# Kernel tuning notes

Hardware: AMD Instinct MI355X
Metric: run time of the kernel (lower is better)

Reference implementation:

```python
import jax, jax.numpy as jnp
import numpy as np

EPS = 1e-7  # keras backend epsilon
ROUTINGS = 3

def squash(s, axis=-1):
    # v = ||s||^2/(1+||s||^2) * s/||s||
    sq = jnp.sum(jnp.square(s), axis=axis, keepdims=True)
    scale = sq / (1.0 + sq) / jnp.sqrt(sq + EPS)
    return scale * s

def setup_inputs() -> dict:
    key = jax.random.key(0)
    k1, k2 = jax.random.split(key)
    B, in_num, in_dim = 64, 2048, 16
    num_caps, dim_caps = 64, 32
    inputs = jax.random.normal(k1, (B, in_num, in_dim), dtype=jnp.float32)
    # glorot_uniform limit = sqrt(6/(fan_in+fan_out)) with fan_in=in_dim, fan_out=dim_caps
    limit = np.sqrt(6.0 / (in_dim + dim_caps)).astype(np.float32)
    W = jax.random.uniform(k2, (num_caps, in_num, dim_caps, in_dim),
                           dtype=jnp.float32, minval=-limit, maxval=limit)
    return {"inputs": inputs, "W": W}

def reference(inputs, W):
    # inputs: [b, i, l]; W: [j, i, k, l]
    # inputs_hat[b, j, i, k] = W[j, i, k, :] @ inputs[b, i, :]
    u_hat = jnp.einsum('jikl,bil->bjik', W, inputs)
    B, J, I, K = u_hat.shape
    b = jnp.zeros((B, J, I), dtype=u_hat.dtype)  # routing logits
    v = None
    for r in range(ROUTINGS):
        c = jax.nn.softmax(b, axis=1)                      # softmax over output capsules j
        s = jnp.einsum('bji,bjik->bjk', c, u_hat)          # weighted sum over input capsules
        v = squash(s)                                      # [b, j, k]
        if r < ROUTINGS - 1:
            b = b + jnp.einsum('bjk,bjik->bji', v, u_hat)  # agreement update
    return v  # [B, num_capsule, dim_capsule]
```

## Files before the change

kernel.cpp:

```cpp
#include <hip/hip_runtime.h>


#define B_ 64
#define I_ 2048
#define L_ 16
#define J_ 64
#define K_ 32
#define N_ 2048

typedef _Float16 half8_t __attribute__((ext_vector_type(8)));
typedef float f32x16 __attribute__((ext_vector_type(16)));
typedef float float4_t __attribute__((ext_vector_type(4)));

__device__ __forceinline__ f32x16 fzero16() {
    f32x16 z;
#pragma unroll
    for (int r = 0; r < 16; ++r) z[r] = 0.f;
    return z;
}

__global__ __launch_bounds__(256) void cast_x_kernel(const float* __restrict__ X,
                                                     _Float16* __restrict__ Xh) {
    unsigned tid = blockIdx.x * 256u + threadIdx.x;
    unsigned b = tid & 63u;
    unsigned i = tid >> 6;
    const float4_t* src = (const float4_t*)(X + (size_t)(b * I_ + i) * L_);
    float4_t f0 = src[0], f1 = src[1], f2 = src[2], f3 = src[3];
    half8_t h0, h1;
#pragma unroll
    for (int e = 0; e < 4; ++e) {
        h0[e] = (_Float16)f0[e];
        h0[4 + e] = (_Float16)f1[e];
        h1[e] = (_Float16)f2[e];
        h1[4 + e] = (_Float16)f3[e];
    }
    _Float16* dst = Xh + (size_t)(i * B_ + b) * L_;
    *(half8_t*)dst = h0;
    *(half8_t*)(dst + 8) = h1;
}

__global__ __launch_bounds__(512) void s0_cast_kernel(const float* __restrict__ Wf,
                                                      _Float16* __restrict__ Wh_out,
                                                      const _Float16* __restrict__ Xh,
                                                      _Float16* __restrict__ parts,
                                                      int SCH, int ICH) {
    const int tid = threadIdx.x;
    const int w = tid >> 6;
    const int l = tid & 63;
    const int h2 = l >> 5;
    const int kb = l & 31;
    const int chunk = blockIdx.x >> 3;
    const int jq = blockIdx.x & 7;
    const int j = jq * 8 + w;

    float s0[16], s1[16];
#pragma unroll
    for (int r = 0; r < 16; ++r) { s0[r] = 0.f; s1[r] = 0.f; }

    const int i0 = chunk * ICH;
    for (int ii = 0; ii < ICH; ++ii) {
        const int i = i0 + ii;
        const _Float16* xb = Xh + (size_t)i * (B_ * L_);
        half8_t xf0 = *(const half8_t*)(xb + kb * L_ + 8 * h2);
        half8_t xf1 = *(const half8_t*)(xb + (32 + kb) * L_ + 8 * h2);
        const float4_t* wsrc =
            (const float4_t*)(Wf + ((size_t)(j * I_ + i) * K_ + kb) * L_ + 8 * h2);
        float4_t a0 = wsrc[0], a1 = wsrc[1];
        half8_t af;
#pragma unroll
        for (int e = 0; e < 4; ++e) {
            af[e] = (_Float16)a0[e];
            af[4 + e] = (_Float16)a1[e];
        }
        *(half8_t*)(Wh_out + ((size_t)(i * J_ + j) * K_ + kb) * L_ + 8 * h2) = af;
        f32x16 acc0 = __builtin_amdgcn_mfma_f32_32x32x16_f16(af, xf0, fzero16(), 0, 0, 0);
        f32x16 acc1 = __builtin_amdgcn_mfma_f32_32x32x16_f16(af, xf1, fzero16(), 0, 0, 0);
#pragma unroll
        for (int r = 0; r < 16; ++r) {
            s0[r] += acc0[r];
            s1[r] += acc1[r];
        }
    }
#pragma unroll
    for (int r = 0; r < 16; ++r) {
        const int k = (r & 3) + 8 * (r >> 2) + 4 * h2;
        _Float16* p = parts + (((size_t)chunk * J_ + j) * K_ + k) * B_;
        p[kb] = (_Float16)s0[r];
        p[32 + kb] = (_Float16)s1[r];
    }
}

__global__ __launch_bounds__(512) void zcalc_kernel(const _Float16* __restrict__ Wh,
                                                    const _Float16* __restrict__ Xh,
                                                    const _Float16* __restrict__ wvz,
                                                    _Float16* __restrict__ ebuf,
                                                    int SCH, int ICH) {
    const int tid = threadIdx.x;
    const int w = tid >> 6;
    const int l = tid & 63;
    const int h2 = l >> 5;
    const int kb = l & 31;
    const int chunk = blockIdx.x >> 3;
    const int jq = blockIdx.x & 7;
    const int j = jq * 8 + w;

    const _Float16* wp = wvz + ((size_t)(j * 2 + h2) * B_ + kb) * 16;
    const half8_t wv00 = *(const half8_t*)wp;
    const half8_t wv01 = *(const half8_t*)(wp + 8);
    const half8_t wv10 = *(const half8_t*)(wp + 512);
    const half8_t wv11 = *(const half8_t*)(wp + 520);

    const int i0 = chunk * ICH;
    for (int ig = 0; ig < ICH; ig += 4) {
        half8_t af[4], x0[4], x1[4];
#pragma unroll
        for (int q = 0; q < 4; ++q) {
            const int i = i0 + ig + q;
            const _Float16* xb = Xh + (size_t)i * (B_ * L_);
            x0[q] = *(const half8_t*)(xb + kb * L_ + 8 * h2);
            x1[q] = *(const half8_t*)(xb + (32 + kb) * L_ + 8 * h2);
            af[q] = *(const half8_t*)(Wh + ((size_t)(i * J_ + j) * K_ + kb) * L_ + 8 * h2);
        }
#pragma unroll
        for (int q = 0; q < 4; ++q) {
            const int i = i0 + ig + q;
            f32x16 acc0 = __builtin_amdgcn_mfma_f32_32x32x16_f16(af[q], x0[q], fzero16(), 0, 0, 0);
            f32x16 acc1 = __builtin_amdgcn_mfma_f32_32x32x16_f16(af[q], x1[q], fzero16(), 0, 0, 0);
            float z0a = 0.f, z0b = 0.f, z0c = 0.f, z0d = 0.f;
            float z1a = 0.f, z1b = 0.f, z1c = 0.f, z1d = 0.f;
#pragma unroll
            for (int r = 0; r < 4; ++r) {
                z0a += acc0[r]      * (float)wv00[r];
                z0b += acc0[r + 4]  * (float)wv00[r + 4];
                z0c += acc0[r + 8]  * (float)wv01[r];
                z0d += acc0[r + 12] * (float)wv01[r + 4];
                z1a += acc1[r]      * (float)wv10[r];
                z1b += acc1[r + 4]  * (float)wv10[r + 4];
                z1c += acc1[r + 8]  * (float)wv11[r];
                z1d += acc1[r + 12] * (float)wv11[r + 4];
            }
            float z0 = (z0a + z0b) + (z0c + z0d);
            float z1 = (z1a + z1b) + (z1c + z1d);
            z0 += __shfl_xor(z0, 32, 64);
            z1 += __shfl_xor(z1, 32, 64);
            const float zf = fminf((l < 32) ? z0 : z1, 11.0f);
            ebuf[((size_t)j * I_ + i) * B_ + l] = (_Float16)__expf(zf);
        }
    }
}

__global__ __launch_bounds__(256) void dsum_kernel(const _Float16* __restrict__ ebuf,
                                                   float* __restrict__ rD) {
    const int w = threadIdx.x >> 6;
    const int l = threadIdx.x & 63;
    const int i = blockIdx.x * 4 + w;
    float p0 = 0.f, p1 = 0.f, p2 = 0.f, p3 = 0.f;
#pragma unroll
    for (int jq = 0; jq < 16; ++jq) {
        p0 += (float)ebuf[((size_t)(jq * 4 + 0) * I_ + i) * B_ + l];
        p1 += (float)ebuf[((size_t)(jq * 4 + 1) * I_ + i) * B_ + l];
        p2 += (float)ebuf[((size_t)(jq * 4 + 2) * I_ + i) * B_ + l];
        p3 += (float)ebuf[((size_t)(jq * 4 + 3) * I_ + i) * B_ + l];
    }
    rD[i * B_ + l] = 1.0f / ((p0 + p1) + (p2 + p3));
}

__global__ __launch_bounds__(512) void s_kernel(const _Float16* __restrict__ Wh,
                                                const _Float16* __restrict__ Xh,
                                                const _Float16* __restrict__ ebuf,
                                                const float* __restrict__ rD,
                                                _Float16* __restrict__ parts,
                                                int SCH, int ICH) {
    const int tid = threadIdx.x;
    const int w = tid >> 6;
    const int l = tid & 63;
    const int h2 = l >> 5;
    const int kb = l & 31;
    const int chunk = blockIdx.x >> 3;
    const int jq = blockIdx.x & 7;
    const int j = jq * 8 + w;

    float s0[16], s1[16];
#pragma unroll
    for (int r = 0; r < 16; ++r) { s0[r] = 0.f; s1[r] = 0.f; }

    const int i0 = chunk * ICH;
    for (int ig = 0; ig < ICH; ig += 4) {
        half8_t af[4], x0[4], x1[4];
        float e0[4], e1[4], d0[4], d1[4];
#pragma unroll
        for (int q = 0; q < 4; ++q) {
            const int i = i0 + ig + q;
            const _Float16* xb = Xh + (size_t)i * (B_ * L_);
            x0[q] = *(const half8_t*)(xb + kb * L_ + 8 * h2);
            x1[q] = *(const half8_t*)(xb + (32 + kb) * L_ + 8 * h2);
            af[q] = *(const half8_t*)(Wh + ((size_t)(i * J_ + j) * K_ + kb) * L_ + 8 * h2);
            const _Float16* ep = ebuf + ((size_t)j * I_ + i) * B_;
            e0[q] = (float)ep[kb];
            e1[q] = (float)ep[32 + kb];
            d0[q] = rD[i * B_ + kb];
            d1[q] = rD[i * B_ + 32 + kb];
        }
#pragma unroll
        for (int q = 0; q < 4; ++q) {
            f32x16 acc0 = __builtin_amdgcn_mfma_f32_32x32x16_f16(af[q], x0[q], fzero16(), 0, 0, 0);
            f32x16 acc1 = __builtin_amdgcn_mfma_f32_32x32x16_f16(af[q], x1[q], fzero16(), 0, 0, 0);
            const float c0 = e0[q] * d0[q];
            const float c1 = e1[q] * d1[q];
#pragma unroll
            for (int r = 0; r < 16; ++r) {
                s0[r] += c0 * acc0[r];
                s1[r] += c1 * acc1[r];
            }
        }
    }
#pragma unroll
    for (int r = 0; r < 16; ++r) {
        const int k = (r & 3) + 8 * (r >> 2) + 4 * h2;
        _Float16* p = parts + (((size_t)chunk * J_ + j) * K_ + k) * B_;
        p[kb] = (_Float16)s0[r];
        p[32 + kb] = (_Float16)s1[r];
    }
}

__global__ __launch_bounds__(512) void reduce_kernel(const _Float16* __restrict__ parts,
                                                     _Float16* __restrict__ wvz,
                                                     float* __restrict__ out,
                                                     int SCH, int STEP) {
    __shared__ float ssql[8][64];
    const int j = blockIdx.x;
    const int t = threadIdx.x;
    const int b = t & 63;
    const int kg = t >> 6;

    float acc[4] = {0.f, 0.f, 0.f, 0.f};
    for (int ch = 0; ch < SCH; ++ch) {
        const _Float16* p = parts + (((size_t)ch * J_ + j) * K_ + kg * 4) * B_ + b;
#pragma unroll
        for (int q = 0; q < 4; ++q) acc[q] += (float)p[(size_t)q * B_];
    }
    if (STEP == 0) {
#pragma unroll
        for (int q = 0; q < 4; ++q) acc[q] *= (1.0f / 64.0f);
    }
    ssql[kg][b] = acc[0] * acc[0] + acc[1] * acc[1] + acc[2] * acc[2] + acc[3] * acc[3];
    __syncthreads();
    float sq = 0.f;
#pragma unroll
    for (int g = 0; g < 8; ++g) sq += ssql[g][b];
    const float scale = sq / (1.0f + sq) / sqrtf(sq + 1e-7f);

    if (STEP == 2) {
#pragma unroll
        for (int q = 0; q < 4; ++q)
            out[(size_t)b * N_ + j * K_ + kg * 4 + q] = acc[q] * scale;
    } else {
        _Float16* wp = wvz + ((size_t)(j * 2 + (kg & 1)) * B_ + b) * 16 + 4 * (kg >> 1);
#pragma unroll
        for (int q = 0; q < 4; ++q) {
            const float prev = (STEP == 0) ? 0.f : (float)wp[q];
            wp[q] = (_Float16)(prev + acc[q] * scale);
        }
    }
}

extern "C" void kernel_launch(void* const* d_in, const int* in_sizes, int n_in,
                              void* d_out, int out_size, void* d_ws, size_t ws_size,
                              hipStream_t stream) {
    const float* X = (const float*)d_in[0];
    const float* W = (const float*)d_in[1];
    float* out = (float*)d_out;
    char* ws = (char*)d_ws;

    const size_t WH_BYTES = (size_t)I_ * J_ * K_ * L_ * 2;
    const size_t XH_BYTES = (size_t)I_ * B_ * L_ * 2;
    const size_t WVZ_BYTES = (size_t)J_ * 2 * B_ * 16 * 2;
    const size_t EB_BYTES = (size_t)J_ * I_ * B_ * 2;
    const size_t RD_BYTES = (size_t)I_ * B_ * 4;
    const size_t FIX = WH_BYTES + XH_BYTES + WVZ_BYTES + EB_BYTES + RD_BYTES;

    int SCH = 64;
    if (ws_size < FIX + (size_t)64 * N_ * B_ * 2) SCH = 32;
    if (ws_size < FIX + (size_t)32 * N_ * B_ * 2) SCH = 16;
    const int ICH = I_ / SCH;

    _Float16* Wh = (_Float16*)ws;
    _Float16* Xh = (_Float16*)(ws + WH_BYTES);
    _Float16* wvz = (_Float16*)(ws + WH_BYTES + XH_BYTES);
    _Float16* ebuf = (_Float16*)(ws + WH_BYTES + XH_BYTES + WVZ_BYTES);
    float* rD = (float*)(ws + WH_BYTES + XH_BYTES + WVZ_BYTES + EB_BYTES);
    _Float16* parts = (_Float16*)(ws + FIX);

    cast_x_kernel<<<dim3((B_ * I_) / 256), dim3(256), 0, stream>>>(X, Xh);

    s0_cast_kernel<<<dim3(SCH * 8), dim3(512), 0, stream>>>(W, Wh, Xh, parts, SCH, ICH);
    reduce_kernel<<<dim3(J_), dim3(512), 0, stream>>>(parts, wvz, out, SCH, 0);

    zcalc_kernel<<<dim3(SCH * 8), dim3(512), 0, stream>>>(Wh, Xh, wvz, ebuf, SCH, ICH);
    dsum_kernel<<<dim3(I_ / 4), dim3(256), 0, stream>>>(ebuf, rD);
    s_kernel<<<dim3(SCH * 8), dim3(512), 0, stream>>>(Wh, Xh, ebuf, rD, parts, SCH, ICH);
    reduce_kernel<<<dim3(J_), dim3(512), 0, stream>>>(parts, wvz, out, SCH, 1);

    zcalc_kernel<<<dim3(SCH * 8), dim3(512), 0, stream>>>(Wh, Xh, wvz, ebuf, SCH, ICH);
    dsum_kernel<<<dim3(I_ / 4), dim3(256), 0, stream>>>(ebuf, rD);
    s_kernel<<<dim3(SCH * 8), dim3(512), 0, stream>>>(Wh, Xh, ebuf, rD, parts, SCH, ICH);
    reduce_kernel<<<dim3(J_), dim3(512), 0, stream>>>(parts, wvz, out, SCH, 2);

    (void)in_sizes; (void)n_in; (void)out_size;
}
```

Baseline: 297.9 us.

## Fuse logit, softmax denominator and normalization into one per-input-block kernel

Replaces the separate zcalc and dsum kernels with one kernel. Each block owns 4 input capsules across all 64 output capsules, keeps exp(logits) in LDS, reduces the softmax denominator there, and writes normalized coefficients c. The s kernel then reads c directly instead of reading e and the reciprocal denominator separately. This removes one launch per routing step, a full re-read of the exp buffer, and the rD buffer traffic, at the cost of a 32KB LDS tile and a different grid shape that may lower occupancy.

```diff
diff --git a/kernel.cpp b/kernel.cpp
--- a/kernel.cpp
+++ b/kernel.cpp
@@ -90,42 +90,41 @@
     }
 }
 
-__global__ __launch_bounds__(512) void zcalc_kernel(const _Float16* __restrict__ Wh,
-                                                    const _Float16* __restrict__ Xh,
-                                                    const _Float16* __restrict__ wvz,
-                                                    _Float16* __restrict__ ebuf,
-                                                    int SCH, int ICH) {
+__global__ __launch_bounds__(512) void zsm2_kernel(const _Float16* __restrict__ Wh,
+                                                   const _Float16* __restrict__ Xh,
+                                                   const _Float16* __restrict__ wvz,
+                                                   _Float16* __restrict__ cbuf) {
+    __shared__ _Float16 elds[J_ * 4 * B_];
+    __shared__ float rdl[4 * B_];
     const int tid = threadIdx.x;
     const int w = tid >> 6;
     const int l = tid & 63;
     const int h2 = l >> 5;
     const int kb = l & 31;
-    const int chunk = blockIdx.x >> 3;
-    const int jq = blockIdx.x & 7;
-    const int j = jq * 8 + w;
-
-    const _Float16* wp = wvz + ((size_t)(j * 2 + h2) * B_ + kb) * 16;
-    const half8_t wv00 = *(const half8_t*)wp;
-    const half8_t wv01 = *(const half8_t*)(wp + 8);
-    const half8_t wv10 = *(const half8_t*)(wp + 512);
-    const half8_t wv11 = *(const half8_t*)(wp + 520);
-
-    const int i0 = chunk * ICH;
-    for (int ig = 0; ig < ICH; ig += 4) {
-        half8_t af[4], x0[4], x1[4];
-#pragma unroll
-        for (int q = 0; q < 4; ++q) {
-            const int i = i0 + ig + q;
-            const _Float16* xb = Xh + (size_t)i * (B_ * L_);
-            x0[q] = *(const half8_t*)(xb + kb * L_ + 8 * h2);
-            x1[q] = *(const half8_t*)(xb + (32 + kb) * L_ + 8 * h2);
-            af[q] = *(const half8_t*)(Wh + ((size_t)(i * J_ + j) * K_ + kb) * L_ + 8 * h2);
-        }
-#pragma unroll
-        for (int q = 0; q < 4; ++q) {
-            const int i = i0 + ig + q;
-            f32x16 acc0 = __builtin_amdgcn_mfma_f32_32x32x16_f16(af[q], x0[q], fzero16(), 0, 0, 0);
-            f32x16 acc1 = __builtin_amdgcn_mfma_f32_32x32x16_f16(af[q], x1[q], fzero16(), 0, 0, 0);
+    const int i0 = blockIdx.x * 4;
+
+    half8_t xf0[4], xf1[4];
+#pragma unroll
+    for (int ii = 0; ii < 4; ++ii) {
+        const _Float16* xb = Xh + (size_t)(i0 + ii) * (B_ * L_);
+        xf0[ii] = *(const half8_t*)(xb + kb * L_ + 8 * h2);
+        xf1[ii] = *(const half8_t*)(xb + (32 + kb) * L_ + 8 * h2);
+    }
+
+#pragma unroll
+    for (int jj = 0; jj < 8; ++jj) {
+        const int j = w * 8 + jj;
+        const _Float16* wp = wvz + ((size_t)(j * 2 + h2) * B_ + kb) * 16;
+        const half8_t wv00 = *(const half8_t*)wp;
+        const half8_t wv01 = *(const half8_t*)(wp + 8);
+        const half8_t wv10 = *(const half8_t*)(wp + 512);
+        const half8_t wv11 = *(const half8_t*)(wp + 520);
+#pragma unroll
+        for (int ii = 0; ii < 4; ++ii) {
+            half8_t af = *(const half8_t*)(Wh +
+                ((size_t)((i0 + ii) * J_ + j) * K_ + kb) * L_ + 8 * h2);
+            f32x16 acc0 = __builtin_amdgcn_mfma_f32_32x32x16_f16(af, xf0[ii], fzero16(), 0, 0, 0);
+            f32x16 acc1 = __builtin_amdgcn_mfma_f32_32x32x16_f16(af, xf1[ii], fzero16(), 0, 0, 0);
             float z0a = 0.f, z0b = 0.f, z0c = 0.f, z0d = 0.f;
             float z1a = 0.f, z1b = 0.f, z1c = 0.f, z1d = 0.f;
 #pragma unroll
@@ -144,31 +143,38 @@
             z0 += __shfl_xor(z0, 32, 64);
             z1 += __shfl_xor(z1, 32, 64);
             const float zf = fminf((l < 32) ? z0 : z1, 11.0f);
-            ebuf[((size_t)j * I_ + i) * B_ + l] = (_Float16)__expf(zf);
-        }
-    }
-}
-
-__global__ __launch_bounds__(256) void dsum_kernel(const _Float16* __restrict__ ebuf,
-                                                   float* __restrict__ rD) {
-    const int w = threadIdx.x >> 6;
-    const int l = threadIdx.x & 63;
-    const int i = blockIdx.x * 4 + w;
-    float p0 = 0.f, p1 = 0.f, p2 = 0.f, p3 = 0.f;
-#pragma unroll
-    for (int jq = 0; jq < 16; ++jq) {
-        p0 += (float)ebuf[((size_t)(jq * 4 + 0) * I_ + i) * B_ + l];
-        p1 += (float)ebuf[((size_t)(jq * 4 + 1) * I_ + i) * B_ + l];
-        p2 += (float)ebuf[((size_t)(jq * 4 + 2) * I_ + i) * B_ + l];
-        p3 += (float)ebuf[((size_t)(jq * 4 + 3) * I_ + i) * B_ + l];
-    }
-    rD[i * B_ + l] = 1.0f / ((p0 + p1) + (p2 + p3));
+            elds[((size_t)j * 4 + ii) * B_ + l] = (_Float16)__expf(zf);
+        }
+    }
+    __syncthreads();
+
+    if (w < 4) {
+        float p0 = 0.f, p1 = 0.f, p2 = 0.f, p3 = 0.f;
+#pragma unroll
+        for (int jq = 0; jq < 16; ++jq) {
+            p0 += (float)elds[((size_t)(jq * 4 + 0) * 4 + w) * B_ + l];
+            p1 += (float)elds[((size_t)(jq * 4 + 1) * 4 + w) * B_ + l];
+            p2 += (float)elds[((size_t)(jq * 4 + 2) * 4 + w) * B_ + l];
+            p3 += (float)elds[((size_t)(jq * 4 + 3) * 4 + w) * B_ + l];
+        }
+        rdl[w * B_ + l] = 1.0f / ((p0 + p1) + (p2 + p3));
+    }
+    __syncthreads();
+
+#pragma unroll
+    for (int jj = 0; jj < 8; ++jj) {
+        const int j = w * 8 + jj;
+#pragma unroll
+        for (int ii = 0; ii < 4; ++ii) {
+            const float c = (float)elds[((size_t)j * 4 + ii) * B_ + l] * rdl[ii * B_ + l];
+            cbuf[((size_t)j * I_ + (i0 + ii)) * B_ + l] = (_Float16)c;
+        }
+    }
 }
 
 __global__ __launch_bounds__(512) void s_kernel(const _Float16* __restrict__ Wh,
                                                 const _Float16* __restrict__ Xh,
-                                                const _Float16* __restrict__ ebuf,
-                                                const float* __restrict__ rD,
+                                                const _Float16* __restrict__ cbuf,
                                                 _Float16* __restrict__ parts,
                                                 int SCH, int ICH) {
     const int tid = threadIdx.x;
@@ -187,7 +193,7 @@
     const int i0 = chunk * ICH;
     for (int ig = 0; ig < ICH; ig += 4) {
         half8_t af[4], x0[4], x1[4];
-        float e0[4], e1[4], d0[4], d1[4];
+        float c0[4], c1[4];
 #pragma unroll
         for (int q = 0; q < 4; ++q) {
             const int i = i0 + ig + q;
@@ -195,22 +201,18 @@
             x0[q] = *(const half8_t*)(xb + kb * L_ + 8 * h2);
             x1[q] = *(const half8_t*)(xb + (32 + kb) * L_ + 8 * h2);
             af[q] = *(const half8_t*)(Wh + ((size_t)(i * J_ + j) * K_ + kb) * L_ + 8 * h2);
-            const _Float16* ep = ebuf + ((size_t)j * I_ + i) * B_;
-            e0[q] = (float)ep[kb];
-            e1[q] = (float)ep[32 + kb];
-            d0[q] = rD[i * B_ + kb];
-            d1[q] = rD[i * B_ + 32 + kb];
+            const _Float16* cp = cbuf + ((size_t)j * I_ + i) * B_;
+            c0[q] = (float)cp[kb];
+            c1[q] = (float)cp[32 + kb];
         }
 #pragma unroll
         for (int q = 0; q < 4; ++q) {
             f32x16 acc0 = __builtin_amdgcn_mfma_f32_32x32x16_f16(af[q], x0[q], fzero16(), 0, 0, 0);
             f32x16 acc1 = __builtin_amdgcn_mfma_f32_32x32x16_f16(af[q], x1[q], fzero16(), 0, 0, 0);
-            const float c0 = e0[q] * d0[q];
-            const float c1 = e1[q] * d1[q];
 #pragma unroll
             for (int r = 0; r < 16; ++r) {
-                s0[r] += c0 * acc0[r];
-                s1[r] += c1 * acc1[r];
+                s0[r] += c0[q] * acc0[r];
+                s1[r] += c1[q] * acc1[r];
             }
         }
     }
@@ -275,9 +277,8 @@
     const size_t WH_BYTES = (size_t)I_ * J_ * K_ * L_ * 2;
     const size_t XH_BYTES = (size_t)I_ * B_ * L_ * 2;
     const size_t WVZ_BYTES = (size_t)J_ * 2 * B_ * 16 * 2;
-    const size_t EB_BYTES = (size_t)J_ * I_ * B_ * 2;
-    const size_t RD_BYTES = (size_t)I_ * B_ * 4;
-    const size_t FIX = WH_BYTES + XH_BYTES + WVZ_BYTES + EB_BYTES + RD_BYTES;
+    const size_t CB_BYTES = (size_t)J_ * I_ * B_ * 2;
+    const size_t FIX = WH_BYTES + XH_BYTES + WVZ_BYTES + CB_BYTES;
 
     int SCH = 64;
     if (ws_size < FIX + (size_t)64 * N_ * B_ * 2) SCH = 32;
@@ -287,8 +288,7 @@
     _Float16* Wh = (_Float16*)ws;
     _Float16* Xh = (_Float16*)(ws + WH_BYTES);
     _Float16* wvz = (_Float16*)(ws + WH_BYTES + XH_BYTES);
-    _Float16* ebuf = (_Float16*)(ws + WH_BYTES + XH_BYTES + WVZ_BYTES);
-    float* rD = (float*)(ws + WH_BYTES + XH_BYTES + WVZ_BYTES + EB_BYTES);
+    _Float16* cbuf = (_Float16*)(ws + WH_BYTES + XH_BYTES + WVZ_BYTES);
     _Float16* parts = (_Float16*)(ws + FIX);
 
     cast_x_kernel<<<dim3((B_ * I_) / 256), dim3(256), 0, stream>>>(X, Xh);
@@ -296,14 +296,12 @@
     s0_cast_kernel<<<dim3(SCH * 8), dim3(512), 0, stream>>>(W, Wh, Xh, parts, SCH, ICH);
     reduce_kernel<<<dim3(J_), dim3(512), 0, stream>>>(parts, wvz, out, SCH, 0);
 
-    zcalc_kernel<<<dim3(SCH * 8), dim3(512), 0, stream>>>(Wh, Xh, wvz, ebuf, SCH, ICH);
-    dsum_kernel<<<dim3(I_ / 4), dim3(256), 0, stream>>>(ebuf, rD);
-    s_kernel<<<dim3(SCH * 8), dim3(512), 0, stream>>>(Wh, Xh, ebuf, rD, parts, SCH, ICH);
+    zsm2_kernel<<<dim3(I_ / 4), dim3(512), 0, stream>>>(Wh, Xh, wvz, cbuf);
+    s_kernel<<<dim3(SCH * 8), dim3(512), 0, stream>>>(Wh, Xh, cbuf, parts, SCH, ICH);
     reduce_kernel<<<dim3(J_), dim3(512), 0, stream>>>(parts, wvz, out, SCH, 1);
 
-    zcalc_kernel<<<dim3(SCH * 8), dim3(512), 0, stream>>>(Wh, Xh, wvz, ebuf, SCH, ICH);
-    dsum_kernel<<<dim3(I_ / 4), dim3(256), 0, stream>>>(ebuf, rD);
-    s_kernel<<<dim3(SCH * 8), dim3(512), 0, stream>>>(Wh, Xh, ebuf, rD, parts, SCH, ICH);
+    zsm2_kernel<<<dim3(I_ / 4), dim3(512), 0, stream>>>(Wh, Xh, wvz, cbuf);
+    s_kernel<<<dim3(SCH * 8), dim3(512), 0, stream>>>(Wh, Xh, cbuf, parts, SCH, ICH);
     reduce_kernel<<<dim3(J_), dim3(512), 0, stream>>>(parts, wvz, out, SCH, 2);
 
     (void)in_sizes; (void)n_in; (void)out_size;
```

Result: slower. 307.4 us (+3.2%).
